# Performance work log

Hardware: AMD Instinct MI355X
Metric: run time of the kernel (lower is better)

## Reference

```python
import jax, jax.numpy as jnp
import numpy as np

NH = 16      # num_heads
EPS = 1e-6   # RMSNorm eps


def rmsnorm(x, w):
    return x * jax.lax.rsqrt(jnp.mean(x * x, axis=-1, keepdims=True) + EPS) * w


def rotate_half(x):
    x1, x2 = jnp.split(x, 2, axis=-1)
    return jnp.concatenate([-x2, x1], axis=-1)


def apply_rope(x, cos, sin):
    # x: [B,H,N,hd]; cos/sin: [N,hd]
    return x * cos + rotate_half(x) * sin


def attention(x, qkv_w, qkv_b, qn_w, kn_w, proj_w, proj_b, cos, sin):
    B, N, C = x.shape
    hd = C // NH
    qkv = (x @ qkv_w.T + qkv_b).reshape(B, N, 3, NH, hd).transpose(2, 0, 3, 1, 4)
    q, k, v = qkv[0], qkv[1], qkv[2]            # [B,H,N,hd]
    q = apply_rope(rmsnorm(q, qn_w), cos, sin)
    k = apply_rope(rmsnorm(k, kn_w), cos, sin)
    scores = jnp.einsum('bhqd,bhkd->bhqk', q, k) / jnp.sqrt(jnp.float32(hd))
    attn = jax.nn.softmax(scores, axis=-1)
    out = jnp.einsum('bhqk,bhkd->bhqd', attn, v)
    out = out.transpose(0, 2, 1, 3).reshape(B, N, C)
    return out @ proj_w.T + proj_b


def jit_block(x, c, cos_s, sin_s, cos_t, sin_t,
              norm1_w, norm2_w, norm3_w,
              qkv_s_w, qkv_s_b, qn_s_w, kn_s_w, proj_s_w, proj_s_b,
              qkv_t_w, qkv_t_b, qn_t_w, kn_t_w, proj_t_w, proj_t_b,
              w12_w, w12_b, w3_w, w3_b, ada_w, ada_b):
    B, T, L, D = x.shape
    mods = (jax.nn.silu(c) @ ada_w.T + ada_b).reshape(B, 9, D)
    sh_s, sc_s, g_s = mods[:, 0], mods[:, 1], mods[:, 2]
    sh_t, sc_t, g_t = mods[:, 3], mods[:, 4], mods[:, 5]
    sh_m, sc_m, g_m = mods[:, 6], mods[:, 7], mods[:, 8]

    # spatial attention over L, batched over B*T
    xs = x.reshape(B * T, L, D)
    sh = jnp.repeat(sh_s, T, axis=0)
    sc = jnp.repeat(sc_s, T, axis=0)
    g = jnp.repeat(g_s, T, axis=0)
    xs_n = rmsnorm(xs, norm1_w) * (1 + sc[:, None, :]) + sh[:, None, :]
    xs = xs + g[:, None, :] * attention(xs_n, qkv_s_w, qkv_s_b, qn_s_w, kn_s_w,
                                        proj_s_w, proj_s_b, cos_s, sin_s)
    x = xs.reshape(B, T, L, D)

    # temporal attention over T, batched over B*L
    xt = x.transpose(0, 2, 1, 3).reshape(B * L, T, D)
    sh = jnp.repeat(sh_t, L, axis=0)
    sc = jnp.repeat(sc_t, L, axis=0)
    g = jnp.repeat(g_t, L, axis=0)
    xt_n = rmsnorm(xt, norm2_w) * (1 + sc[:, None, :]) + sh[:, None, :]
    xt = xt + g[:, None, :] * attention(xt_n, qkv_t_w, qkv_t_b, qn_t_w, kn_t_w,
                                        proj_t_w, proj_t_b, cos_t, sin_t)
    x = xt.reshape(B, L, T, D).transpose(0, 2, 1, 3)

    # SwiGLU FFN with adaLN modulation + gate
    x_n = rmsnorm(x, norm3_w) * (1 + sc_m[:, None, None, :]) + sh_m[:, None, None, :]
    h12 = x_n @ w12_w.T + w12_b
    h1, h2 = jnp.split(h12, 2, axis=-1)
    mlp_out = (jax.nn.silu(h1) * h2) @ w3_w.T + w3_b
    return x + g_m[:, None, None, :] * mlp_out


def _rope_tables(n, hd):
    inv = 1.0 / (10000.0 ** (np.arange(0, hd, 2, dtype=np.float64) / hd))
    ang = np.arange(n, dtype=np.float64)[:, None] * inv[None, :]
    cos = np.concatenate([np.cos(ang), np.cos(ang)], -1).astype(np.float32)
    sin = np.concatenate([np.sin(ang), np.sin(ang)], -1).astype(np.float32)
    return jnp.asarray(cos), jnp.asarray(sin)


def setup_inputs() -> dict:
    key = jax.random.key(0)
    B, T, L, D = 2, 16, 256, 1024
    HD = D // NH
    HFF = int(int(D * 4.0) * 2 / 3)  # 2730
    ks = jax.random.split(key, 16)
    s = 0.02
    cos_s, sin_s = _rope_tables(L, HD)
    cos_t, sin_t = _rope_tables(T, HD)
    return {
        'x': jax.random.normal(ks[0], (B, T, L, D), jnp.float32),
        'c': jax.random.normal(ks[1], (B, D), jnp.float32),
        'cos_s': cos_s, 'sin_s': sin_s, 'cos_t': cos_t, 'sin_t': sin_t,
        'norm1_w': jnp.ones((D,), jnp.float32),
        'norm2_w': jnp.ones((D,), jnp.float32),
        'norm3_w': jnp.ones((D,), jnp.float32),
        'qkv_s_w': jax.random.normal(ks[2], (3 * D, D), jnp.float32) * s,
        'qkv_s_b': jnp.zeros((3 * D,), jnp.float32),
        'qn_s_w': jnp.ones((HD,), jnp.float32),
        'kn_s_w': jnp.ones((HD,), jnp.float32),
        'proj_s_w': jax.random.normal(ks[3], (D, D), jnp.float32) * s,
        'proj_s_b': jnp.zeros((D,), jnp.float32),
        'qkv_t_w': jax.random.normal(ks[4], (3 * D, D), jnp.float32) * s,
        'qkv_t_b': jnp.zeros((3 * D,), jnp.float32),
        'qn_t_w': jnp.ones((HD,), jnp.float32),
        'kn_t_w': jnp.ones((HD,), jnp.float32),
        'proj_t_w': jax.random.normal(ks[5], (D, D), jnp.float32) * s,
        'proj_t_b': jnp.zeros((D,), jnp.float32),
        'w12_w': jax.random.normal(ks[6], (2 * HFF, D), jnp.float32) * s,
        'w12_b': jnp.zeros((2 * HFF,), jnp.float32),
        'w3_w': jax.random.normal(ks[7], (D, HFF), jnp.float32) * s,
        'w3_b': jnp.zeros((D,), jnp.float32),
        'ada_w': jax.random.normal(ks[8], (9 * D, D), jnp.float32) * s,
        'ada_b': jnp.zeros((9 * D,), jnp.float32),
    }


def reference(x, c, cos_s, sin_s, cos_t, sin_t,
              norm1_w, norm2_w, norm3_w,
              qkv_s_w, qkv_s_b, qn_s_w, kn_s_w, proj_s_w, proj_s_b,
              qkv_t_w, qkv_t_b, qn_t_w, kn_t_w, proj_t_w, proj_t_b,
              w12_w, w12_b, w3_w, w3_b, ada_w, ada_b):
    return jit_block(x, c, cos_s, sin_s, cos_t, sin_t,
                     norm1_w, norm2_w, norm3_w,
                     qkv_s_w, qkv_s_b, qn_s_w, kn_s_w, proj_s_w, proj_s_b,
                     qkv_t_w, qkv_t_b, qn_t_w, kn_t_w, proj_t_w, proj_t_b,
                     w12_w, w12_b, w3_w, w3_b, ada_w, ada_b)
```

## Files before the change

kernel.cpp:

```cpp
#include <hip/hip_runtime.h>
#include <cstdint>
#include <cstddef>

typedef unsigned short u16;
typedef __attribute__((ext_vector_type(8))) short short8;
typedef __attribute__((ext_vector_type(4))) float f32x4;

__device__ __forceinline__ float bf2f(u16 u) {
  union { uint32_t u; float f; } x; x.u = ((uint32_t)u) << 16; return x.f;
}
__device__ __forceinline__ u16 f2bf(float f) {
  union { float f; uint32_t u; } x; x.f = f;
  uint32_t r = x.u + 0x7FFFu + ((x.u >> 16) & 1u);
  return (u16)(r >> 16);
}
__device__ __forceinline__ float silu_f(float x) { return x / (1.f + __expf(-x)); }

__device__ __forceinline__ void glds16(const u16* g, u16* l) {
  __builtin_amdgcn_global_load_lds(
      (const __attribute__((address_space(1))) void*)g,
      (__attribute__((address_space(3))) void*)l, 16, 0, 0);
}

#define MFMA16 __builtin_amdgcn_mfma_f32_16x16x32_bf16

__device__ __forceinline__ void wg_barrier() {
  asm volatile("" ::: "memory");
  __builtin_amdgcn_s_barrier();
  asm volatile("" ::: "memory");
}

__global__ void cvt_pad_kernel(const float* __restrict__ in, u16* __restrict__ out,
                               int cols_out, int rows_in, int cols_in, int row_off, int total) {
  int i = blockIdx.x * 256 + threadIdx.x;
  if (i >= total) return;
  int r = i / cols_out, ci = i - r * cols_out;
  float v = 0.f;
  if (r < rows_in && ci < cols_in) v = in[(size_t)(r + row_off) * cols_in + ci];
  out[i] = f2bf(v);
}

__global__ void mods_kernel(const float* __restrict__ c, const float* __restrict__ ada_w,
                            const float* __restrict__ ada_b, float* __restrict__ mods) {
  int j = blockIdx.x * 4 + (threadIdx.x >> 6);
  int lane = threadIdx.x & 63;
  float a0 = 0.f, a1 = 0.f;
  for (int k = lane; k < 1024; k += 64) {
    float w = ada_w[(size_t)j * 1024 + k];
    a0 += silu_f(c[k]) * w;
    a1 += silu_f(c[1024 + k]) * w;
  }
  #pragma unroll
  for (int off = 32; off > 0; off >>= 1) { a0 += __shfl_down(a0, off); a1 += __shfl_down(a1, off); }
  if (lane == 0) {
    float bb = ada_b[j];
    mods[j] = a0 + bb;
    mods[9216 + j] = a1 + bb;
  }
}

__global__ __launch_bounds__(256) void norm_mod_kernel(
    const float* __restrict__ X, u16* __restrict__ Y,
    const float* __restrict__ nw, const float* __restrict__ mods,
    int sh_idx, int transpose) {
  int row = blockIdx.x;
  int b = row >> 12;
  int in_row;
  if (transpose) { int rem = row & 4095; int l = rem >> 4, t = rem & 15; in_row = (b << 12) + (t << 8) + l; }
  else in_row = row;
  int tid = threadIdx.x;
  float4 v = ((const float4*)(X + (size_t)in_row * 1024))[tid];
  float ss = v.x * v.x + v.y * v.y + v.z * v.z + v.w * v.w;
  #pragma unroll
  for (int off = 32; off > 0; off >>= 1) ss += __shfl_down(ss, off);
  __shared__ float red[4];
  if ((tid & 63) == 0) red[tid >> 6] = ss;
  __syncthreads();
  float rms = rsqrtf((red[0] + red[1] + red[2] + red[3]) * (1.f / 1024.f) + 1e-6f);
  const float* mb = mods + (size_t)b * 9216 + (size_t)sh_idx * 1024;
  float4 sh = ((const float4*)mb)[tid];
  float4 sc = ((const float4*)(mb + 1024))[tid];
  float4 w  = ((const float4*)nw)[tid];
  ushort4 o;
  o.x = f2bf(v.x * rms * w.x * (1.f + sc.x) + sh.x);
  o.y = f2bf(v.y * rms * w.y * (1.f + sc.y) + sh.y);
  o.z = f2bf(v.z * rms * w.z * (1.f + sc.z) + sh.z);
  o.w = f2bf(v.w * rms * w.w * (1.f + sc.w) + sh.w);
  ((ushort4*)(Y + (size_t)row * 1024))[tid] = o;
}

#define CHK2(b, s) (((b) * 4 + (s)) << 13)
#define CHK3(b, s) (((b) * 3 + (s)) << 13)

__device__ __forceinline__ void stage_half(const u16* __restrict__ gp, int ldk,
                                           int row_base, int k0,
                                           u16* Sbase, int slot_u16,
                                           int wid, int srow, int scol) {
  #pragma unroll
  for (int c = 0; c < 2; c++) {
    int row = c * 64 + wid * 8 + srow;
    glds16(gp + (size_t)(row_base + row) * ldk + (k0 + scol),
           Sbase + slot_u16 + c * 4096 + wid * 512);
  }
}

template<int MODE>
__global__ __launch_bounds__(512, 2) void gemm256_n128(
    const u16* __restrict__ A, const u16* __restrict__ W,
    const float* __restrict__ bias, void* __restrict__ Cv,
    int K, int ldc,
    const float* __restrict__ base, const float* __restrict__ mods, int gidx) {
  __shared__ u16 S[49152];
  const int tid = threadIdx.x, wid = tid >> 6, lane = tid & 63;
  const int wm = wid >> 1, wn = wid & 1;
  const int quad = lane >> 4, r = lane & 15;
  const int bid = blockIdx.x, xcd = bid & 7, l = bid >> 3;
  const int mt = (xcd << 2) | (l & 3), nt = l >> 2;
  const int m0 = mt * 256, n0 = nt * 128;

  const int srow = lane >> 3;
  const int scol = ((lane & 7) ^ srow) << 3;
  const int kx0 = (quad * 8) ^ ((r & 7) << 3);
  const int kx1 = (32 + quad * 8) ^ ((r & 7) << 3);
  const int aslot = wm >> 1;
  const int arow = ((wm & 1) * 64 + r) * 64;
  const int brow = (wn * 64 + r) * 64;

  f32x4 zero = {0.f, 0.f, 0.f, 0.f};
  f32x4 acc[4][4];
  #pragma unroll
  for (int i = 0; i < 4; i++)
    #pragma unroll
    for (int j = 0; j < 4; j++) acc[i][j] = zero;
  short8 fA[4][2], fB[4][2];

  const int nk = K >> 6;

  stage_half(A, K, m0,       0, S, CHK3(0,0), wid, srow, scol);
  stage_half(A, K, m0 + 128, 0, S, CHK3(0,1), wid, srow, scol);
  stage_half(W, K, n0,       0, S, CHK3(0,2), wid, srow, scol);
  if (nk > 1) {
    stage_half(A, K, m0,       64, S, CHK3(1,0), wid, srow, scol);
    stage_half(A, K, m0 + 128, 64, S, CHK3(1,1), wid, srow, scol);
    stage_half(W, K, n0,       64, S, CHK3(1,2), wid, srow, scol);
    asm volatile("s_waitcnt vmcnt(6)" ::: "memory");
  } else {
    asm volatile("s_waitcnt vmcnt(0)" ::: "memory");
  }
  __builtin_amdgcn_s_barrier();

  for (int u = 0; u < nk; ++u) {
    const int cur = u & 1;
    const int k2 = (u + 2) << 6;
    const int s1 = (u + 1 < nk), s2 = (u + 2 < nk);
    const u16* cA = S + CHK3(cur, aslot);
    const u16* cB = S + CHK3(cur, 2);
    u16* bcur = S + CHK3(cur, 0);

    #pragma unroll
    for (int f = 0; f < 4; f++) {
      fA[f][0] = *(const short8*)(cA + arow + f * 1024 + kx0);
      fA[f][1] = *(const short8*)(cA + arow + f * 1024 + kx1);
    }
    #pragma unroll
    for (int j = 0; j < 4; j++) {
      fB[j][0] = *(const short8*)(cB + brow + j * 1024 + kx0);
      fB[j][1] = *(const short8*)(cB + brow + j * 1024 + kx1);
    }
    wg_barrier();

    if (s2) {
      stage_half(A, K, m0,       k2, bcur, 0 << 13, wid, srow, scol);
      stage_half(A, K, m0 + 128, k2, bcur, 1 << 13, wid, srow, scol);
      stage_half(W, K, n0,       k2, bcur, 2 << 13, wid, srow, scol);
    }
    __builtin_amdgcn_s_setprio(1);
    #pragma unroll
    for (int f = 0; f < 4; f++)
      #pragma unroll
      for (int j = 0; j < 4; j++) {
        acc[f][j] = MFMA16(fA[f][0], fB[j][0], acc[f][j], 0, 0, 0);
        acc[f][j] = MFMA16(fA[f][1], fB[j][1], acc[f][j], 0, 0, 0);
      }
    __builtin_amdgcn_s_setprio(0);
    if (s2)      asm volatile("s_waitcnt vmcnt(6)" ::: "memory");
    else if (s1) asm volatile("s_waitcnt vmcnt(0)" ::: "memory");
    wg_barrier();
  }

  float* Cf = (float*)Cv;
  u16* Ch = (u16*)Cv;
  #pragma unroll
  for (int f = 0; f < 4; f++) {
    int row = m0 + wm * 64 + f * 16 + quad * 4;
    #pragma unroll
    for (int j = 0; j < 4; j++) {
      int col = n0 + wn * 64 + j * 16 + r;
      float bv = bias[col];
      #pragma unroll
      for (int rr = 0; rr < 4; rr++) {
        int ri = row + rr;
        float vv = acc[f][j][rr] + bv;
        if (MODE == 0) {
          Cf[(size_t)ri * ldc + col] = vv;
        } else if (MODE == 1) {
          Ch[(size_t)ri * ldc + col] = f2bf(vv);
        } else {
          int ro = ri;
          if (MODE == 3) { int rem = ri & 4095; ro = (ri & ~4095) + ((rem & 15) << 8) + (rem >> 4); }
          int b = ri >> 12;
          float g = mods[(size_t)b * 9216 + (size_t)gidx * 1024 + col];
          Cf[(size_t)ro * 1024 + col] = base[(size_t)ro * 1024 + col] + g * vv;
        }
      }
    }
  }
}

__global__ __launch_bounds__(512, 2) void gemm256_w12(
    const u16* __restrict__ A, const u16* __restrict__ W1, const u16* __restrict__ W2,
    const float* __restrict__ bias, u16* __restrict__ Hb) {
  __shared__ u16 S[65536];
  const int tid = threadIdx.x, wid = tid >> 6, lane = tid & 63;
  const int wm = wid >> 2, wn = wid & 3;
  const int quad = lane >> 4, r = lane & 15;
  const int bid = blockIdx.x, xcd = bid & 7, l = bid >> 3;
  const int mt = (xcd << 2) | (l & 3), nt = l >> 2;
  const int m0 = mt * 256, n0 = nt * 128;

  const int srow = lane >> 3;
  const int scol = ((lane & 7) ^ srow) << 3;
  const int kx0 = (quad * 8) ^ ((r & 7) << 3);
  const int kx1 = (32 + quad * 8) ^ ((r & 7) << 3);
  const int arow = (wm * 64 + r) * 64;
  const int brow = (wn * 32 + r) * 64;
  const int K = 1024, nk = 16;

  f32x4 zero = {0.f, 0.f, 0.f, 0.f};
  f32x4 acc1[8][2], acc2[8][2];
  #pragma unroll
  for (int i = 0; i < 8; i++)
    #pragma unroll
    for (int j = 0; j < 2; j++) { acc1[i][j] = zero; acc2[i][j] = zero; }
  short8 fA[4][2], fW1[2][2], fW2[2][2];

  stage_half(A,  K, m0,       0, S, CHK2(0,0), wid, srow, scol);
  stage_half(W1, K, n0,       0, S, CHK2(0,2), wid, srow, scol);
  stage_half(W2, K, n0,       0, S, CHK2(0,3), wid, srow, scol);
  stage_half(A,  K, m0 + 128, 0, S, CHK2(0,1), wid, srow, scol);
  stage_half(A,  K, m0,      64, S, CHK2(1,0), wid, srow, scol);
  stage_half(W1, K, n0,      64, S, CHK2(1,2), wid, srow, scol);
  stage_half(W2, K, n0,      64, S, CHK2(1,3), wid, srow, scol);
  stage_half(A,  K, m0 + 128,64, S, CHK2(1,1), wid, srow, scol);
  asm volatile("s_waitcnt vmcnt(8)" ::: "memory");
  __builtin_amdgcn_s_barrier();

  for (int u = 0; u < nk; ++u) {
    const int cur = u & 1;
    const int k2 = (u + 2) << 6;
    const int s1 = (u + 1 < nk), s2 = (u + 2 < nk);
    const u16* cA0 = S + CHK2(cur, 0);
    const u16* cA1 = S + CHK2(cur, 1);
    const u16* cW1 = S + CHK2(cur, 2);
    const u16* cW2 = S + CHK2(cur, 3);
    u16* bcur = S + CHK2(cur, 0);

    #pragma unroll
    for (int f = 0; f < 4; f++) {
      fA[f][0] = *(const short8*)(cA0 + arow + f * 1024 + kx0);
      fA[f][1] = *(const short8*)(cA0 + arow + f * 1024 + kx1);
    }
    #pragma unroll
    for (int j = 0; j < 2; j++) {
      fW1[j][0] = *(const short8*)(cW1 + brow + j * 1024 + kx0);
      fW1[j][1] = *(const short8*)(cW1 + brow + j * 1024 + kx1);
      fW2[j][0] = *(const short8*)(cW2 + brow + j * 1024 + kx0);
      fW2[j][1] = *(const short8*)(cW2 + brow + j * 1024 + kx1);
    }
    wg_barrier();

    if (s2) {
      stage_half(A,  K, m0, k2, bcur, 0 << 13, wid, srow, scol);
      stage_half(W1, K, n0, k2, bcur, 2 << 13, wid, srow, scol);
      stage_half(W2, K, n0, k2, bcur, 3 << 13, wid, srow, scol);
    }
    __builtin_amdgcn_s_setprio(1);
    #pragma unroll
    for (int f = 0; f < 4; f++)
      #pragma unroll
      for (int j = 0; j < 2; j++) {
        acc1[f][j] = MFMA16(fA[f][0], fW1[j][0], acc1[f][j], 0, 0, 0);
        acc1[f][j] = MFMA16(fA[f][1], fW1[j][1], acc1[f][j], 0, 0, 0);
        acc2[f][j] = MFMA16(fA[f][0], fW2[j][0], acc2[f][j], 0, 0, 0);
        acc2[f][j] = MFMA16(fA[f][1], fW2[j][1], acc2[f][j], 0, 0, 0);
      }
    __builtin_amdgcn_s_setprio(0);
    #pragma unroll
    for (int f = 0; f < 4; f++) {
      fA[f][0] = *(const short8*)(cA1 + arow + f * 1024 + kx0);
      fA[f][1] = *(const short8*)(cA1 + arow + f * 1024 + kx1);
    }
    wg_barrier();

    if (s2) stage_half(A, K, m0 + 128, k2, bcur, 1 << 13, wid, srow, scol);
    __builtin_amdgcn_s_setprio(1);
    #pragma unroll
    for (int f = 0; f < 4; f++)
      #pragma unroll
      for (int j = 0; j < 2; j++) {
        acc1[4 + f][j] = MFMA16(fA[f][0], fW1[j][0], acc1[4 + f][j], 0, 0, 0);
        acc1[4 + f][j] = MFMA16(fA[f][1], fW1[j][1], acc1[4 + f][j], 0, 0, 0);
        acc2[4 + f][j] = MFMA16(fA[f][0], fW2[j][0], acc2[4 + f][j], 0, 0, 0);
        acc2[4 + f][j] = MFMA16(fA[f][1], fW2[j][1], acc2[4 + f][j], 0, 0, 0);
      }
    __builtin_amdgcn_s_setprio(0);
    if (s2)      asm volatile("s_waitcnt vmcnt(8)" ::: "memory");
    else if (s1) asm volatile("s_waitcnt vmcnt(0)" ::: "memory");
    wg_barrier();
  }

  #pragma unroll
  for (int f = 0; f < 8; f++) {
    int row = m0 + (f >> 2) * 128 + wm * 64 + (f & 3) * 16 + quad * 4;
    #pragma unroll
    for (int j = 0; j < 2; j++) {
      int col = n0 + wn * 32 + j * 16 + r;
      float b1 = (col < 2730) ? bias[col] : 0.f;
      float b2 = (col < 2730) ? bias[2730 + col] : 0.f;
      #pragma unroll
      for (int rr = 0; rr < 4; rr++) {
        float h1 = acc1[f][j][rr] + b1;
        float h2 = acc2[f][j][rr] + b2;
        Hb[(size_t)(row + rr) * 2816 + col] = f2bf(silu_f(h1) * h2);
      }
    }
  }
}

#define KSS 72
#define VSS 264
#define PSS 40
__global__ __launch_bounds__(256) void attn_s_mfma(
    const u16* __restrict__ QKV,
    const float* __restrict__ qn_w, const float* __restrict__ kn_w,
    const float* __restrict__ cosT, const float* __restrict__ sinT,
    u16* __restrict__ AO) {
  __shared__ u16 Ks[256 * KSS];
  __shared__ u16 Vt[64 * VSS];
  __shared__ u16 Pl[4 * 32 * PSS];
  int pair = blockIdx.x;
  int s = pair >> 4, h = pair & 15;
  int qhalf = blockIdx.y;
  int tid = threadIdx.x, wid = tid >> 6, lane = tid & 63;
  int quad = lane >> 4, r = lane & 15;

  {
    int j = tid;
    size_t rowb = ((size_t)(s * 256 + j)) * 3072 + (size_t)h * 64;
    const short8* kr = (const short8*)(QKV + rowb + 1024);
    float xk[64]; float ssq = 0.f;
    #pragma unroll
    for (int cg = 0; cg < 8; cg++) {
      short8 kk = kr[cg];
      #pragma unroll
      for (int e = 0; e < 8; e++) { float v = bf2f((u16)kk[e]); xk[cg * 8 + e] = v; ssq += v * v; }
    }
    float rms = rsqrtf(ssq * (1.f / 64.f) + 1e-6f);
    short8 kq[8];
    #pragma unroll
    for (int d = 0; d < 32; d++) {
      float a = xk[d] * rms * kn_w[d];
      float b2 = xk[d + 32] * rms * kn_w[d + 32];
      u16 o0 = f2bf(a * cosT[j * 64 + d] - b2 * sinT[j * 64 + d]);
      u16 o1 = f2bf(b2 * cosT[j * 64 + 32 + d] + a * sinT[j * 64 + 32 + d]);
      kq[d >> 3][d & 7] = (short)o0;
      kq[(d + 32) >> 3][d & 7] = (short)o1;
    }
    #pragma unroll
    for (int cg = 0; cg < 8; cg++) *(short8*)(Ks + j * KSS + cg * 8) = kq[cg];
    const short8* vr = (const short8*)(QKV + rowb + 2048);
    #pragma unroll
    for (int cg = 0; cg < 8; cg++) {
      short8 vv = vr[cg];
      #pragma unroll
      for (int e = 0; e < 8; e++) Vt[(cg * 8 + e) * VSS + j] = (u16)vv[e];
    }
  }

  int qbase = qhalf * 128 + wid * 32;
  short8 qa[2][2];
  float lrow[2][4];
  {
    float qv[2][2][8];
    float ssq[2] = {0.f, 0.f};
    #pragma unroll
    for (int i = 0; i < 2; i++) {
      int grow = s * 256 + qbase + i * 16 + r;
      #pragma unroll
      for (int kk = 0; kk < 2; kk++) {
        short8 qraw = *(const short8*)(QKV + (size_t)grow * 3072 + h * 64 + kk * 32 + quad * 8);
        #pragma unroll
        for (int e = 0; e < 8; e++) { float v = bf2f((u16)qraw[e]); qv[i][kk][e] = v; ssq[i] += v * v; }
      }
    }
    #pragma unroll
    for (int i = 0; i < 2; i++) {
      float sv = ssq[i];
      sv += __shfl_xor(sv, 16);
      sv += __shfl_xor(sv, 32);
      float rms = rsqrtf(sv * (1.f / 64.f) + 1e-6f);
      int qrow = qbase + i * 16 + r;
      #pragma unroll
      for (int e = 0; e < 8; e++) {
        int d0 = quad * 8 + e;
        float a = qv[i][0][e] * rms * qn_w[d0];
        float b2 = qv[i][1][e] * rms * qn_w[d0 + 32];
        qa[i][0][e] = (short)f2bf(a * cosT[qrow * 64 + d0] - b2 * sinT[qrow * 64 + d0]);
        qa[i][1][e] = (short)f2bf(b2 * cosT[qrow * 64 + 32 + d0] + a * sinT[qrow * 64 + 32 + d0]);
      }
    }
  }
  __syncthreads();

  f32x4 zero = {0.f, 0.f, 0.f, 0.f};
  f32x4 acc[2][16];
  #pragma unroll
  for (int i = 0; i < 2; i++)
    #pragma unroll
    for (int j = 0; j < 16; j++) acc[i][j] = zero;
  #pragma unroll
  for (int kk = 0; kk < 2; kk++) {
    #pragma unroll
    for (int j = 0; j < 16; j++) {
      short8 bfr = *(const short8*)(Ks + (j * 16 + r) * KSS + kk * 32 + quad * 8);
      acc[0][j] = MFMA16(qa[0][kk], bfr, acc[0][j], 0, 0, 0);
      acc[1][j] = MFMA16(qa[1][kk], bfr, acc[1][j], 0, 0, 0);
    }
  }

  #pragma unroll
  for (int i = 0; i < 2; i++) {
    #pragma unroll
    for (int rr = 0; rr < 4; rr++) {
      float mx = acc[i][0][rr];
      #pragma unroll
      for (int j = 1; j < 16; j++) mx = fmaxf(mx, acc[i][j][rr]);
      #pragma unroll
      for (int msk = 1; msk < 16; msk <<= 1) mx = fmaxf(mx, __shfl_xor(mx, msk));
      float ls = 0.f;
      #pragma unroll
      for (int j = 0; j < 16; j++) { float p = __expf((acc[i][j][rr] - mx) * 0.125f); acc[i][j][rr] = p; ls += p; }
      #pragma unroll
      for (int msk = 1; msk < 16; msk <<= 1) ls += __shfl_xor(ls, msk);
      lrow[i][rr] = ls;
    }
  }

  f32x4 oacc[2][4];
  #pragma unroll
  for (int i = 0; i < 2; i++)
    #pragma unroll
    for (int j = 0; j < 4; j++) oacc[i][j] = zero;
  u16* plw = Pl + wid * 32 * PSS;
  #pragma unroll
  for (int kk = 0; kk < 8; kk++) {
    #pragma unroll
    for (int i = 0; i < 2; i++)
      #pragma unroll
      for (int jj = 0; jj < 2; jj++) {
        int j = kk * 2 + jj;
        #pragma unroll
        for (int rr = 0; rr < 4; rr++)
          plw[(i * 16 + quad * 4 + rr) * PSS + jj * 16 + r] = f2bf(acc[i][j][rr]);
      }
    short8 pa0 = *(const short8*)(plw + r * PSS + quad * 8);
    short8 pa1 = *(const short8*)(plw + (16 + r) * PSS + quad * 8);
    #pragma unroll
    for (int j4 = 0; j4 < 4; j4++) {
      short8 vfr = *(const short8*)(Vt + (j4 * 16 + r) * VSS + kk * 32 + quad * 8);
      oacc[0][j4] = MFMA16(pa0, vfr, oacc[0][j4], 0, 0, 0);
      oacc[1][j4] = MFMA16(pa1, vfr, oacc[1][j4], 0, 0, 0);
    }
  }

  #pragma unroll
  for (int i = 0; i < 2; i++) {
    #pragma unroll
    for (int rr = 0; rr < 4; rr++) {
      float inv = 1.f / lrow[i][rr];
      int row = s * 256 + qbase + i * 16 + quad * 4 + rr;
      #pragma unroll
      for (int j4 = 0; j4 < 4; j4++)
        AO[(size_t)row * 1024 + h * 64 + j4 * 16 + r] = f2bf(oacc[i][j4][rr] * inv);
    }
  }
}

__global__ __launch_bounds__(256) void attn_t_kernel(
    const u16* __restrict__ QKV,
    const float* __restrict__ qn_w, const float* __restrict__ kn_w,
    const float* __restrict__ cosT, const float* __restrict__ sinT,
    u16* __restrict__ AO) {
  __shared__ u16 kb[256 * 64];
  __shared__ u16 vb[256 * 64];
  int bl = blockIdx.x;
  int tid = threadIdx.x;
  int h = tid >> 4, t = tid & 15;
  size_t rowbase = ((size_t)(bl * 16 + t)) * 3072;
  int slot = h * 16 + t;
  {
    const u16* kr = QKV + rowbase + 1024 + h * 64;
    float xk[64]; float ss = 0.f;
    #pragma unroll
    for (int d = 0; d < 64; d++) { xk[d] = bf2f(kr[d]); ss += xk[d] * xk[d]; }
    float rms = rsqrtf(ss * (1.f / 64.f) + 1e-6f);
    #pragma unroll
    for (int d = 0; d < 64; d++) xk[d] *= rms * kn_w[d];
    #pragma unroll
    for (int d = 0; d < 32; d++) {
      float a = xk[d], bb = xk[d + 32];
      kb[slot * 64 + d]      = f2bf(a * cosT[t * 64 + d]       - bb * sinT[t * 64 + d]);
      kb[slot * 64 + 32 + d] = f2bf(bb * cosT[t * 64 + 32 + d] + a * sinT[t * 64 + 32 + d]);
    }
    const u16* vr = QKV + rowbase + 2048 + h * 64;
    #pragma unroll
    for (int d = 0; d < 64; d++) vb[slot * 64 + d] = vr[d];
  }
  float q[64];
  {
    const u16* qr = QKV + rowbase + h * 64;
    float ss = 0.f;
    #pragma unroll
    for (int d = 0; d < 64; d++) { q[d] = bf2f(qr[d]); ss += q[d] * q[d]; }
    float rms = rsqrtf(ss * (1.f / 64.f) + 1e-6f);
    #pragma unroll
    for (int d = 0; d < 64; d++) q[d] *= rms * qn_w[d];
    #pragma unroll
    for (int d = 0; d < 32; d++) {
      float a = q[d], bb = q[d + 32];
      q[d]      = a * cosT[t * 64 + d]       - bb * sinT[t * 64 + d];
      q[d + 32] = bb * cosT[t * 64 + 32 + d] + a * sinT[t * 64 + 32 + d];
    }
  }
  __syncthreads();
  float scv[16]; float mx = -1e30f;
  #pragma unroll
  for (int j = 0; j < 16; j++) {
    float sc = 0.f;
    const short8* krow = (const short8*)(kb + (h * 16 + j) * 64);
    #pragma unroll
    for (int vv = 0; vv < 8; vv++) {
      short8 kk = krow[vv];
      #pragma unroll
      for (int e = 0; e < 8; e++) sc += q[vv * 8 + e] * bf2f((u16)kk[e]);
    }
    scv[j] = sc * 0.125f;
    mx = fmaxf(mx, scv[j]);
  }
  float ssum = 0.f;
  #pragma unroll
  for (int j = 0; j < 16; j++) { scv[j] = __expf(scv[j] - mx); ssum += scv[j]; }
  float inv = 1.f / ssum;
  float o[64];
  #pragma unroll
  for (int d = 0; d < 64; d++) o[d] = 0.f;
  #pragma unroll
  for (int j = 0; j < 16; j++) {
    const short8* vrow = (const short8*)(vb + (h * 16 + j) * 64);
    #pragma unroll
    for (int vv = 0; vv < 8; vv++) {
      short8 vk = vrow[vv];
      #pragma unroll
      for (int e = 0; e < 8; e++) o[vv * 8 + e] += scv[j] * bf2f((u16)vk[e]);
    }
  }
  u16* op = AO + ((size_t)(bl * 16 + t)) * 1024 + h * 64;
  #pragma unroll
  for (int d = 0; d < 64; d++) op[d] = f2bf(o[d] * inv);
}

extern "C" void kernel_launch(void* const* d_in, const int* in_sizes, int n_in,
                              void* d_out, int out_size, void* d_ws, size_t ws_size,
                              hipStream_t stream) {
  const float* x        = (const float*)d_in[0];
  const float* c        = (const float*)d_in[1];
  const float* cos_s    = (const float*)d_in[2];
  const float* sin_s    = (const float*)d_in[3];
  const float* cos_t    = (const float*)d_in[4];
  const float* sin_t    = (const float*)d_in[5];
  const float* norm1w   = (const float*)d_in[6];
  const float* norm2w   = (const float*)d_in[7];
  const float* norm3w   = (const float*)d_in[8];
  const float* qkv_s_w  = (const float*)d_in[9];
  const float* qkv_s_b  = (const float*)d_in[10];
  const float* qn_s_w   = (const float*)d_in[11];
  const float* kn_s_w   = (const float*)d_in[12];
  const float* proj_s_w = (const float*)d_in[13];
  const float* proj_s_b = (const float*)d_in[14];
  const float* qkv_t_w  = (const float*)d_in[15];
  const float* qkv_t_b  = (const float*)d_in[16];
  const float* qn_t_w   = (const float*)d_in[17];
  const float* kn_t_w   = (const float*)d_in[18];
  const float* proj_t_w = (const float*)d_in[19];
  const float* proj_t_b = (const float*)d_in[20];
  const float* w12_w    = (const float*)d_in[21];
  const float* w12_b    = (const float*)d_in[22];
  const float* w3_w     = (const float*)d_in[23];
  const float* w3_b     = (const float*)d_in[24];
  const float* ada_w    = (const float*)d_in[25];
  const float* ada_b    = (const float*)d_in[26];
  float* out = (float*)d_out;

  char* wsp = (char*)d_ws;
  size_t off = 0;
  auto alloc = [&](size_t bytes) { size_t p = off; off += (bytes + 255) & ~(size_t)255; return p; };
  float* modsb = (float*)(wsp + alloc(2 * 9216 * 4));
  u16*   BIG   = (u16*)  (wsp + alloc((size_t)8192 * 3072 * 2));
  char*  XnP   = (char*) (wsp + alloc((size_t)8192 * 1024 * 4));
  u16*   AO    = (u16*)  (wsp + alloc((size_t)8192 * 1024 * 2));
  u16*   Wq    = (u16*)  (wsp + alloc((size_t)3072 * 1024 * 2));
  u16*   Wp    = (u16*)  (wsp + alloc((size_t)2816 * 1024 * 2));
  u16*   W3b   = (u16*)  (wsp + alloc((size_t)1024 * 2816 * 2));
  u16* W1p = Wq;
  u16* W2p = Wp;
  u16* Xn  = (u16*)XnP;
  float* Xcur = out;

  dim3 blk(256);
  dim3 blk512(512);
  int tot;
  mods_kernel<<<2304, blk, 0, stream>>>(c, ada_w, ada_b, modsb);

  tot = 3072 * 1024; cvt_pad_kernel<<<(tot + 255) / 256, blk, 0, stream>>>(qkv_s_w, Wq, 1024, 3072, 1024, 0, tot);
  tot = 1024 * 1024; cvt_pad_kernel<<<(tot + 255) / 256, blk, 0, stream>>>(proj_s_w, Wp, 1024, 1024, 1024, 0, tot);
  norm_mod_kernel<<<8192, blk, 0, stream>>>(x, Xn, norm1w, modsb, 0, 0);
  gemm256_n128<1><<<dim3(32 * 24), blk512, 0, stream>>>(Xn, Wq, qkv_s_b, BIG, 1024, 3072, nullptr, nullptr, 0);
  attn_s_mfma<<<dim3(512, 2), blk, 0, stream>>>(BIG, qn_s_w, kn_s_w, cos_s, sin_s, AO);
  gemm256_n128<2><<<dim3(32 * 8), blk512, 0, stream>>>(AO, Wp, proj_s_b, Xcur, 1024, 1024, x, modsb, 2);

  tot = 3072 * 1024; cvt_pad_kernel<<<(tot + 255) / 256, blk, 0, stream>>>(qkv_t_w, Wq, 1024, 3072, 1024, 0, tot);
  tot = 1024 * 1024; cvt_pad_kernel<<<(tot + 255) / 256, blk, 0, stream>>>(proj_t_w, Wp, 1024, 1024, 1024, 0, tot);
  norm_mod_kernel<<<8192, blk, 0, stream>>>(Xcur, Xn, norm2w, modsb, 3, 1);
  gemm256_n128<1><<<dim3(32 * 24), blk512, 0, stream>>>(Xn, Wq, qkv_t_b, BIG, 1024, 3072, nullptr, nullptr, 0);
  attn_t_kernel<<<512, blk, 0, stream>>>(BIG, qn_t_w, kn_t_w, cos_t, sin_t, AO);
  gemm256_n128<3><<<dim3(32 * 8), blk512, 0, stream>>>(AO, Wp, proj_t_b, Xcur, 1024, 1024, Xcur, modsb, 5);

  tot = 2816 * 1024; cvt_pad_kernel<<<(tot + 255) / 256, blk, 0, stream>>>(w12_w, W1p, 1024, 2730, 1024, 0, tot);
  tot = 2816 * 1024; cvt_pad_kernel<<<(tot + 255) / 256, blk, 0, stream>>>(w12_w, W2p, 1024, 2730, 1024, 2730, tot);
  tot = 1024 * 2816; cvt_pad_kernel<<<(tot + 255) / 256, blk, 0, stream>>>(w3_w, W3b, 2816, 1024, 2730, 0, tot);
  norm_mod_kernel<<<8192, blk, 0, stream>>>(Xcur, Xn, norm3w, modsb, 6, 0);
  gemm256_w12<<<dim3(32 * 22), blk512, 0, stream>>>(Xn, W1p, W2p, w12_b, BIG);
  gemm256_n128<2><<<dim3(32 * 8), blk512, 0, stream>>>(BIG, W3b, w3_b, out, 2816, 1024, Xcur, modsb, 8);
}
```

Baseline: 707.6 us.

## Merge weight conversion launches, precompute GEMM load pointers, widen spatial attention blocks

Replaces the five per-weight fp32-to-bf16 conversion launches with fused kernels: a vectorized float4 converter for qkv+proj and a single kernel for the padded FFN weights. In both GEMM kernels, the per-iteration stage_half address computation is replaced by precomputed global pointers that are advanced by 64 each step and fed straight to global_load_lds. Spatial attention now runs one 512-thread block per (s,h) pair instead of two 256-thread blocks split by query half. K and V staging is divided across the two thread halves, so K/V are loaded once per pair rather than twice. Fewer, larger blocks may reduce occupancy and latency hiding.

```diff
diff --git a/kernel.cpp b/kernel.cpp
--- a/kernel.cpp
+++ b/kernel.cpp
@@ -30,14 +30,33 @@
   asm volatile("" ::: "memory");
 }
 
-__global__ void cvt_pad_kernel(const float* __restrict__ in, u16* __restrict__ out,
-                               int cols_out, int rows_in, int cols_in, int row_off, int total) {
+__global__ void cvt2_kernel(const float* __restrict__ in0, u16* __restrict__ out0, int n0,
+                            const float* __restrict__ in1, u16* __restrict__ out1, int n1) {
+  int i = (blockIdx.x * 256 + threadIdx.x) * 4;
+  const float* in; u16* out;
+  if (i < n0) { in = in0 + i; out = out0 + i; }
+  else { i -= n0; if (i >= n1) return; in = in1 + i; out = out1 + i; }
+  float4 v = *(const float4*)in;
+  ushort4 o; o.x = f2bf(v.x); o.y = f2bf(v.y); o.z = f2bf(v.z); o.w = f2bf(v.w);
+  *(ushort4*)out = o;
+}
+
+__global__ void cvt3_kernel(const float* __restrict__ w12, u16* __restrict__ W1, u16* __restrict__ W2,
+                            const float* __restrict__ w3, u16* __restrict__ W3) {
   int i = blockIdx.x * 256 + threadIdx.x;
-  if (i >= total) return;
-  int r = i / cols_out, ci = i - r * cols_out;
-  float v = 0.f;
-  if (r < rows_in && ci < cols_in) v = in[(size_t)(r + row_off) * cols_in + ci];
-  out[i] = f2bf(v);
+  const int n1 = 2816 * 1024;
+  const int n3 = 1024 * 2816;
+  if (i < n1) {
+    int r = i >> 10, c = i & 1023;
+    W1[i] = f2bf(r < 2730 ? w12[(size_t)r * 1024 + c] : 0.f);
+  } else if (i < 2 * n1) {
+    int j = i - n1; int r = j >> 10, c = j & 1023;
+    W2[j] = f2bf(r < 2730 ? w12[(size_t)(r + 2730) * 1024 + c] : 0.f);
+  } else {
+    int j = i - 2 * n1; if (j >= n3) return;
+    int r = j / 2816, c = j - r * 2816;
+    W3[j] = f2bf(c < 2730 ? w3[(size_t)r * 2730 + c] : 0.f);
+  }
 }
 
 __global__ void mods_kernel(const float* __restrict__ c, const float* __restrict__ ada_w,
@@ -136,6 +155,13 @@
 
   const int nk = K >> 6;
 
+  const u16* gA0c0 = A + (size_t)(m0 +       wid * 8 + srow) * K + scol + 128;
+  const u16* gA0c1 = A + (size_t)(m0 +  64 + wid * 8 + srow) * K + scol + 128;
+  const u16* gA1c0 = A + (size_t)(m0 + 128 + wid * 8 + srow) * K + scol + 128;
+  const u16* gA1c1 = A + (size_t)(m0 + 192 + wid * 8 + srow) * K + scol + 128;
+  const u16* gBc0  = W + (size_t)(n0 +       wid * 8 + srow) * K + scol + 128;
+  const u16* gBc1  = W + (size_t)(n0 +  64 + wid * 8 + srow) * K + scol + 128;
+
   stage_half(A, K, m0,       0, S, CHK3(0,0), wid, srow, scol);
   stage_half(A, K, m0 + 128, 0, S, CHK3(0,1), wid, srow, scol);
   stage_half(W, K, n0,       0, S, CHK3(0,2), wid, srow, scol);
@@ -151,11 +177,9 @@
 
   for (int u = 0; u < nk; ++u) {
     const int cur = u & 1;
-    const int k2 = (u + 2) << 6;
     const int s1 = (u + 1 < nk), s2 = (u + 2 < nk);
     const u16* cA = S + CHK3(cur, aslot);
     const u16* cB = S + CHK3(cur, 2);
-    u16* bcur = S + CHK3(cur, 0);
 
     #pragma unroll
     for (int f = 0; f < 4; f++) {
@@ -170,10 +194,12 @@
     wg_barrier();
 
     if (s2) {
-      stage_half(A, K, m0,       k2, bcur, 0 << 13, wid, srow, scol);
-      stage_half(A, K, m0 + 128, k2, bcur, 1 << 13, wid, srow, scol);
-      stage_half(W, K, n0,       k2, bcur, 2 << 13, wid, srow, scol);
-    }
+      u16* Sb = S + cur * 24576 + wid * 512;
+      glds16(gA0c0, Sb);          glds16(gA0c1, Sb + 4096);
+      glds16(gA1c0, Sb + 8192);   glds16(gA1c1, Sb + 12288);
+      glds16(gBc0,  Sb + 16384);  glds16(gBc1,  Sb + 20480);
+    }
+    gA0c0 += 64; gA0c1 += 64; gA1c0 += 64; gA1c1 += 64; gBc0 += 64; gBc1 += 64;
     __builtin_amdgcn_s_setprio(1);
     #pragma unroll
     for (int f = 0; f < 4; f++)
@@ -244,6 +270,15 @@
     for (int j = 0; j < 2; j++) { acc1[i][j] = zero; acc2[i][j] = zero; }
   short8 fA[4][2], fW1[2][2], fW2[2][2];
 
+  const u16* gA0c0 = A  + (size_t)(m0 +       wid * 8 + srow) * K + scol + 128;
+  const u16* gA0c1 = A  + (size_t)(m0 +  64 + wid * 8 + srow) * K + scol + 128;
+  const u16* gA1c0 = A  + (size_t)(m0 + 128 + wid * 8 + srow) * K + scol + 128;
+  const u16* gA1c1 = A  + (size_t)(m0 + 192 + wid * 8 + srow) * K + scol + 128;
+  const u16* gW1c0 = W1 + (size_t)(n0 +       wid * 8 + srow) * K + scol + 128;
+  const u16* gW1c1 = W1 + (size_t)(n0 +  64 + wid * 8 + srow) * K + scol + 128;
+  const u16* gW2c0 = W2 + (size_t)(n0 +       wid * 8 + srow) * K + scol + 128;
+  const u16* gW2c1 = W2 + (size_t)(n0 +  64 + wid * 8 + srow) * K + scol + 128;
+
   stage_half(A,  K, m0,       0, S, CHK2(0,0), wid, srow, scol);
   stage_half(W1, K, n0,       0, S, CHK2(0,2), wid, srow, scol);
   stage_half(W2, K, n0,       0, S, CHK2(0,3), wid, srow, scol);
@@ -257,13 +292,12 @@
 
   for (int u = 0; u < nk; ++u) {
     const int cur = u & 1;
-    const int k2 = (u + 2) << 6;
     const int s1 = (u + 1 < nk), s2 = (u + 2 < nk);
     const u16* cA0 = S + CHK2(cur, 0);
     const u16* cA1 = S + CHK2(cur, 1);
     const u16* cW1 = S + CHK2(cur, 2);
     const u16* cW2 = S + CHK2(cur, 3);
-    u16* bcur = S + CHK2(cur, 0);
+    u16* Sb = S + cur * 32768 + wid * 512;
 
     #pragma unroll
     for (int f = 0; f < 4; f++) {
@@ -280,9 +314,9 @@
     wg_barrier();
 
     if (s2) {
-      stage_half(A,  K, m0, k2, bcur, 0 << 13, wid, srow, scol);
-      stage_half(W1, K, n0, k2, bcur, 2 << 13, wid, srow, scol);
-      stage_half(W2, K, n0, k2, bcur, 3 << 13, wid, srow, scol);
+      glds16(gA0c0, Sb);          glds16(gA0c1, Sb + 4096);
+      glds16(gW1c0, Sb + 16384);  glds16(gW1c1, Sb + 20480);
+      glds16(gW2c0, Sb + 24576);  glds16(gW2c1, Sb + 28672);
     }
     __builtin_amdgcn_s_setprio(1);
     #pragma unroll
@@ -302,7 +336,9 @@
     }
     wg_barrier();
 
-    if (s2) stage_half(A, K, m0 + 128, k2, bcur, 1 << 13, wid, srow, scol);
+    if (s2) { glds16(gA1c0, Sb + 8192); glds16(gA1c1, Sb + 12288); }
+    gA0c0 += 64; gA0c1 += 64; gA1c0 += 64; gA1c1 += 64;
+    gW1c0 += 64; gW1c1 += 64; gW2c0 += 64; gW2c1 += 64;
     __builtin_amdgcn_s_setprio(1);
     #pragma unroll
     for (int f = 0; f < 4; f++)
@@ -340,21 +376,20 @@
 #define KSS 72
 #define VSS 264
 #define PSS 40
-__global__ __launch_bounds__(256) void attn_s_mfma(
+__global__ __launch_bounds__(512) void attn_s_mfma(
     const u16* __restrict__ QKV,
     const float* __restrict__ qn_w, const float* __restrict__ kn_w,
     const float* __restrict__ cosT, const float* __restrict__ sinT,
     u16* __restrict__ AO) {
   __shared__ u16 Ks[256 * KSS];
   __shared__ u16 Vt[64 * VSS];
-  __shared__ u16 Pl[4 * 32 * PSS];
+  __shared__ u16 Pl[8 * 32 * PSS];
   int pair = blockIdx.x;
   int s = pair >> 4, h = pair & 15;
-  int qhalf = blockIdx.y;
   int tid = threadIdx.x, wid = tid >> 6, lane = tid & 63;
   int quad = lane >> 4, r = lane & 15;
 
-  {
+  if (tid < 256) {
     int j = tid;
     size_t rowb = ((size_t)(s * 256 + j)) * 3072 + (size_t)h * 64;
     const short8* kr = (const short8*)(QKV + rowb + 1024);
@@ -378,6 +413,9 @@
     }
     #pragma unroll
     for (int cg = 0; cg < 8; cg++) *(short8*)(Ks + j * KSS + cg * 8) = kq[cg];
+  } else {
+    int j = tid - 256;
+    size_t rowb = ((size_t)(s * 256 + j)) * 3072 + (size_t)h * 64;
     const short8* vr = (const short8*)(QKV + rowb + 2048);
     #pragma unroll
     for (int cg = 0; cg < 8; cg++) {
@@ -387,7 +425,7 @@
     }
   }
 
-  int qbase = qhalf * 128 + wid * 32;
+  int qbase = wid * 32;
   short8 qa[2][2];
   float lrow[2][4];
   {
@@ -628,26 +666,30 @@
 
   dim3 blk(256);
   dim3 blk512(512);
-  int tot;
   mods_kernel<<<2304, blk, 0, stream>>>(c, ada_w, ada_b, modsb);
 
-  tot = 3072 * 1024; cvt_pad_kernel<<<(tot + 255) / 256, blk, 0, stream>>>(qkv_s_w, Wq, 1024, 3072, 1024, 0, tot);
-  tot = 1024 * 1024; cvt_pad_kernel<<<(tot + 255) / 256, blk, 0, stream>>>(proj_s_w, Wp, 1024, 1024, 1024, 0, tot);
+  {
+    int n0 = 3072 * 1024, n1 = 1024 * 1024;
+    cvt2_kernel<<<(n0 + n1) / 1024, blk, 0, stream>>>(qkv_s_w, Wq, n0, proj_s_w, Wp, n1);
+  }
   norm_mod_kernel<<<8192, blk, 0, stream>>>(x, Xn, norm1w, modsb, 0, 0);
   gemm256_n128<1><<<dim3(32 * 24), blk512, 0, stream>>>(Xn, Wq, qkv_s_b, BIG, 1024, 3072, nullptr, nullptr, 0);
-  attn_s_mfma<<<dim3(512, 2), blk, 0, stream>>>(BIG, qn_s_w, kn_s_w, cos_s, sin_s, AO);
+  attn_s_mfma<<<dim3(512), blk512, 0, stream>>>(BIG, qn_s_w, kn_s_w, cos_s, sin_s, AO);
   gemm256_n128<2><<<dim3(32 * 8), blk512, 0, stream>>>(AO, Wp, proj_s_b, Xcur, 1024, 1024, x, modsb, 2);
 
-  tot = 3072 * 1024; cvt_pad_kernel<<<(tot + 255) / 256, blk, 0, stream>>>(qkv_t_w, Wq, 1024, 3072, 1024, 0, tot);
-  tot = 1024 * 1024; cvt_pad_kernel<<<(tot + 255) / 256, blk, 0, stream>>>(proj_t_w, Wp, 1024, 1024, 1024, 0, tot);
+  {
+    int n0 = 3072 * 1024, n1 = 1024 * 1024;
+    cvt2_kernel<<<(n0 + n1) / 1024, blk, 0, stream>>>(qkv_t_w, Wq, n0, proj_t_w, Wp, n1);
+  }
   norm_mod_kernel<<<8192, blk, 0, stream>>>(Xcur, Xn, norm2w, modsb, 3, 1);
   gemm256_n128<1><<<dim3(32 * 24), blk512, 0, stream>>>(Xn, Wq, qkv_t_b, BIG, 1024, 3072, nullptr, nullptr, 0);
   attn_t_kernel<<<512, blk, 0, stream>>>(BIG, qn_t_w, kn_t_w, cos_t, sin_t, AO);
   gemm256_n128<3><<<dim3(32 * 8), blk512, 0, stream>>>(AO, Wp, proj_t_b, Xcur, 1024, 1024, Xcur, modsb, 5);
 
-  tot = 2816 * 1024; cvt_pad_kernel<<<(tot + 255) / 256, blk, 0, stream>>>(w12_w, W1p, 1024, 2730, 1024, 0, tot);
-  tot = 2816 * 1024; cvt_pad_kernel<<<(tot + 255) / 256, blk, 0, stream>>>(w12_w, W2p, 1024, 2730, 1024, 2730, tot);
-  tot = 1024 * 2816; cvt_pad_kernel<<<(tot + 255) / 256, blk, 0, stream>>>(w3_w, W3b, 2816, 1024, 2730, 0, tot);
+  {
+    int tot = 2 * 2816 * 1024 + 1024 * 2816;
+    cvt3_kernel<<<(tot + 255) / 256, blk, 0, stream>>>(w12_w, W1p, W2p, w3_w, W3b);
+  }
   norm_mod_kernel<<<8192, blk, 0, stream>>>(Xcur, Xn, norm3w, modsb, 6, 0);
   gemm256_w12<<<dim3(32 * 22), blk512, 0, stream>>>(Xn, W1p, W2p, w12_b, BIG);
   gemm256_n128<2><<<dim3(32 * 8), blk512, 0, stream>>>(BIG, W3b, w3_b, out, 2816, 1024, Xcur, modsb, 8);
```

Result: faster. 663.1 us (-6.3%).
